# Performance work log

Measured on AMD Instinct MI355X. Metric: run time of the kernel, lower is better.

Reference implementation:

```python
import jax, jax.numpy as jnp
import numpy as np
from jax import lax

CURRICULUM_EP = 12
LI, LS, LW = 0.5, 0.8, 3.0


def _gauss_win(ws, C, dtype):
    coords = jnp.arange(ws, dtype=jnp.float32) - ws // 2
    g = jnp.exp(-coords ** 2 / (2 * 1.5 ** 2))
    win = g[None, :] * g[:, None]
    win = win / win.sum()
    # depthwise kernel, OIHW with I=1, O=C
    return jnp.broadcast_to(win[None, None], (C, 1, ws, ws)).astype(dtype)


def _dwconv(x, win, p, C):
    return lax.conv_general_dilated(
        x, win, window_strides=(1, 1), padding=[(p, p), (p, p)],
        dimension_numbers=('NCHW', 'OIHW', 'NCHW'), feature_group_count=C)


def diff_ssim(x, y, ws=11):
    C1, C2 = 0.01 ** 2, 0.03 ** 2
    C = x.shape[1]
    p = ws // 2
    win = _gauss_win(ws, C, x.dtype)
    mx = _dwconv(x, win, p, C)
    my = _dwconv(y, win, p, C)
    sxx = _dwconv(x * x, win, p, C) - mx ** 2
    syy = _dwconv(y * y, win, p, C) - my ** 2
    sxy = _dwconv(x * y, win, p, C) - mx * my
    ssim_map = (2 * mx * my + C1) * (2 * sxy + C2) / ((mx ** 2 + my ** 2 + C1) * (sxx + syy + C2))
    return ssim_map.mean()


def setup_inputs() -> dict:
    key = jax.random.key(0)
    k1, k2, k3, k4 = jax.random.split(key, 4)
    B, C, H, W = 16, 3, 512, 512
    NB = 1024  # watermark bits
    eps = 1e-4
    cover = jax.random.uniform(k1, (B, C, H, W), dtype=jnp.float32)
    wmed = jax.random.uniform(k2, (B, C, H, W), dtype=jnp.float32)
    wm_orig = jax.random.uniform(k3, (B, NB), dtype=jnp.float32)
    wm_ext = jnp.clip(jax.random.uniform(k4, (B, NB), dtype=jnp.float32), eps, 1.0 - eps)
    return {"cover": cover, "wmed": wmed, "wm_orig": wm_orig, "wm_ext": wm_ext, "epoch": 20}


def reference(cover, wmed, wm_orig, wm_ext, epoch):
    ml = jnp.mean((wmed - cover) ** 2)
    sv = diff_ssim(wmed, cover)
    sl = 1.0 - sv
    wl = jnp.mean(-(wm_orig * jnp.log(wm_ext) + (1.0 - wm_orig) * jnp.log(1.0 - wm_ext)))
    if epoch <= CURRICULUM_EP:
        w_img, w_ssim = 0.05, 0.05
    else:
        progress = min(1.0, (epoch - CURRICULUM_EP) / 10.0)
        w_img = 0.05 + (LI - 0.05) * progress
        w_ssim = 0.05 + (LS - 0.05) * progress
    total = w_img * ml + w_ssim * sl + LW * wl
    return (total, ml, sv, wl)
```

## Files before the change

### kernel.cpp

```cpp
#include <hip/hip_runtime.h>
#include <math.h>

#define H_IMG 512
#define W_IMG 512
#define TH 32
#define TW 32
#define HALO 5
#define WS11 11
#define SH (TH + 2*HALO)
#define NTHREADS 256
#define TPB 4

#define RS 36
#define RBUF_N (5*SH*RS)

typedef float f2 __attribute__((ext_vector_type(2)));

__host__ __device__ constexpr float WT(int t) {
    return (t==0||t==10) ? 0.00102838f :
           (t==1||t==9)  ? 0.00759873f :
           (t==2||t==8)  ? 0.03600075f :
           (t==3||t==7)  ? 0.10936070f :
           (t==4||t==6)  ? 0.21300556f :
           (t==5)        ? 0.26601172f : 0.0f;
}

static __device__ __forceinline__ f2 splat2(float v) { f2 r = {v, v}; return r; }

__global__ __launch_bounds__(NTHREADS, 4) void ssim_mse_tile(
        const float* __restrict__ cover, const float* __restrict__ wmed,
        float* __restrict__ part, int nParts) {
    __shared__ __align__(16) float rbuf[RBUF_N];
    __shared__ float red[8];

    const int tid = threadIdx.x;
    float ssim_acc = 0.f, mse_acc = 0.f;

    for (int it = 0; it < TPB; ++it) {
        const int tile = blockIdx.x * TPB + it;
        const int bx = tile & 15;
        const int by = (tile >> 4) & 15;
        const int pl = tile >> 8;
        const size_t pbase = (size_t)pl * (H_IMG*W_IMG);
        const float* xp = wmed + pbase;
        const float* yp = cover + pbase;
        const int ty0 = by*TH - HALO;
        const int tx0 = bx*TW - HALO;
        const bool xin = (bx != 0) && (bx != 15);

        for (int t = tid; t < SH*8; t += NTHREADS) {
            const int r = t >> 3, c0 = (t & 7) << 2;
            const int gy = ty0 + r;
            const bool rok = (unsigned)gy < (unsigned)H_IMG;
            float xv[14], yv[14];
            if (rok && xin) {
                const int ga = tx0 + c0 - 3;
                const float* rx = xp + (size_t)gy*W_IMG + ga;
                const float* ry = yp + (size_t)gy*W_IMG + ga;
                float4 XA = *(const float4*)(rx);
                float4 XB = *(const float4*)(rx + 4);
                float4 XC = *(const float4*)(rx + 8);
                float4 XD = *(const float4*)(rx + 12);
                float  XE = rx[16];
                float4 YA = *(const float4*)(ry);
                float4 YB = *(const float4*)(ry + 4);
                float4 YC = *(const float4*)(ry + 8);
                float4 YD = *(const float4*)(ry + 12);
                float  YE = ry[16];
                xv[0]=XA.w;  xv[1]=XB.x;  xv[2]=XB.y;  xv[3]=XB.z;  xv[4]=XB.w;
                xv[5]=XC.x;  xv[6]=XC.y;  xv[7]=XC.z;  xv[8]=XC.w;  xv[9]=XD.x;
                xv[10]=XD.y; xv[11]=XD.z; xv[12]=XD.w; xv[13]=XE;
                yv[0]=YA.w;  yv[1]=YB.x;  yv[2]=YB.y;  yv[3]=YB.z;  yv[4]=YB.w;
                yv[5]=YC.x;  yv[6]=YC.y;  yv[7]=YC.z;  yv[8]=YC.w;  yv[9]=YD.x;
                yv[10]=YD.y; yv[11]=YD.z; yv[12]=YD.w; yv[13]=YE;
            } else if (rok) {
                const int gc = tx0 + c0;
                const float* prx = xp + (size_t)gy*W_IMG + gc;
                const float* pry = yp + (size_t)gy*W_IMG + gc;
#pragma unroll
                for (int j = 0; j < 14; ++j) {
                    bool ok = (unsigned)(gc + j) < (unsigned)W_IMG;
                    xv[j] = ok ? prx[j] : 0.f;
                    yv[j] = ok ? pry[j] : 0.f;
                }
            } else {
#pragma unroll
                for (int j = 0; j < 14; ++j) { xv[j] = 0.f; yv[j] = 0.f; }
            }

            if (rok && r >= HALO && r < HALO+TH) {
#pragma unroll
                for (int j = 5; j < 9; ++j) {
                    float d = xv[j] - yv[j];
                    mse_acc = fmaf(d, d, mse_acc);
                }
            }

            f2 A[5][2];
#pragma unroll
            for (int f = 0; f < 5; ++f) { A[f][0] = splat2(0.f); A[f][1] = splat2(0.f); }
#pragma unroll
            for (int j = 0; j < 14; ++j) {
                float px = xv[j], py = yv[j];
                float pxx = px*px, pyy = py*py, pxy = px*py;
#pragma unroll
                for (int p = 0; p < 2; ++p) {
                    const int t0 = j - 2*p;
                    if (t0 >= 0 && t0 <= WS11) {
                        const f2 wp = {WT(t0), WT(t0-1)};
                        A[0][p] = __builtin_elementwise_fma(wp, splat2(px),  A[0][p]);
                        A[1][p] = __builtin_elementwise_fma(wp, splat2(py),  A[1][p]);
                        A[2][p] = __builtin_elementwise_fma(wp, splat2(pxx), A[2][p]);
                        A[3][p] = __builtin_elementwise_fma(wp, splat2(pyy), A[3][p]);
                        A[4][p] = __builtin_elementwise_fma(wp, splat2(pxy), A[4][p]);
                    }
                }
            }
            float* wb = &rbuf[r*RS + c0];
#pragma unroll
            for (int f = 0; f < 5; ++f) {
                *(float4*)(wb + f*SH*RS) =
                    make_float4(A[f][0].x, A[f][0].y, A[f][1].x, A[f][1].y);
            }
        }
        __syncthreads();

        if (((tid >> 7) & 1) == (it & 1)) {
            const f2 c1 = {0.01f*0.01f, 0.01f*0.01f};
            const f2 c2 = {0.03f*0.03f, 0.03f*0.03f};
            const f2 two = {2.f, 2.f};
            const int s  = tid & 127;
            const int c  = s & 31;
            const int r0 = (s >> 5) << 3;
            f2 acc2[5][4];
#pragma unroll
            for (int f = 0; f < 5; ++f)
#pragma unroll
                for (int p = 0; p < 4; ++p) acc2[f][p] = splat2(0.f);
#pragma unroll
            for (int f = 0; f < 5; ++f) {
                const float* rb = &rbuf[f*SH*RS + r0*RS + c];
#pragma unroll
                for (int i = 0; i < 18; ++i) {
                    float v = rb[i*RS];
#pragma unroll
                    for (int p = 0; p < 4; ++p) {
                        const int t0 = i - 2*p;
                        if (t0 >= 0 && t0 <= WS11) {
                            const f2 wp = {WT(t0), WT(t0-1)};
                            acc2[f][p] = __builtin_elementwise_fma(wp, splat2(v), acc2[f][p]);
                        }
                    }
                }
            }
#pragma unroll
            for (int p = 0; p < 4; ++p) {
                f2 mx = acc2[0][p], my = acc2[1][p];
                f2 sxx = acc2[2][p] - mx*mx;
                f2 syy = acc2[3][p] - my*my;
                f2 sxy = acc2[4][p] - mx*my;
                f2 num = (two*mx*my + c1) * (two*sxy + c2);
                f2 den = (mx*mx + my*my + c1) * (sxx + syy + c2);
                ssim_acc += __fdividef(num.x, den.x) + __fdividef(num.y, den.y);
            }
        }
        __syncthreads();
    }

#pragma unroll
    for (int off = 32; off > 0; off >>= 1) {
        ssim_acc += __shfl_down(ssim_acc, off);
        mse_acc  += __shfl_down(mse_acc, off);
    }
    int wid = tid >> 6, lane = tid & 63;
    if (lane == 0) { red[wid] = ssim_acc; red[4+wid] = mse_acc; }
    __syncthreads();
    if (tid == 0) {
        float s = red[0]+red[1]+red[2]+red[3];
        float m = red[4]+red[5]+red[6]+red[7];
        part[blockIdx.x] = s;
        part[nParts + blockIdx.x] = m;
    }
}

#define FT 1024
__global__ __launch_bounds__(FT) void finalize_k(
        const float* __restrict__ part, int nParts,
        const float* __restrict__ wm_orig, const float* __restrict__ wm_ext,
        int nWm, const int* __restrict__ epoch_p,
        float* __restrict__ out, double inv_npix, double inv_nwm) {
    __shared__ double red[48];
    int tid = threadIdx.x;
    double s_ssim = 0.0, s_mse = 0.0, s_wl = 0.0;
    const float4* s4 = (const float4*)part;
    const float4* m4 = (const float4*)(part + nParts);
    int n4 = nParts >> 2;
    for (int i = tid; i < n4; i += FT) {
        float4 v = s4[i];
        s_ssim += (double)((v.x + v.y) + (v.z + v.w));
        float4 u = m4[i];
        s_mse  += (double)((u.x + u.y) + (u.z + u.w));
    }
    const float4* p4 = (const float4*)wm_orig;
    const float4* q4 = (const float4*)wm_ext;
    int w4 = nWm >> 2;
    for (int i = tid; i < w4; i += FT) {
        float4 p = p4[i], q = q4[i];
        float a;
        a  = -(p.x*__logf(q.x) + (1.f-p.x)*__logf(1.f-q.x));
        a += -(p.y*__logf(q.y) + (1.f-p.y)*__logf(1.f-q.y));
        a += -(p.z*__logf(q.z) + (1.f-p.z)*__logf(1.f-q.z));
        a += -(p.w*__logf(q.w) + (1.f-p.w)*__logf(1.f-q.w));
        s_wl += (double)a;
    }
#pragma unroll
    for (int off = 32; off > 0; off >>= 1) {
        s_ssim += __shfl_down(s_ssim, off);
        s_mse  += __shfl_down(s_mse, off);
        s_wl   += __shfl_down(s_wl, off);
    }
    int wid = tid >> 6, lane = tid & 63;
    if (lane == 0) { red[wid] = s_ssim; red[16+wid] = s_mse; red[32+wid] = s_wl; }
    __syncthreads();
    if (tid == 0) {
        double ssim_sum = 0.0, mse_sum = 0.0, wl_sum = 0.0;
        for (int i = 0; i < 16; ++i) {
            ssim_sum += red[i]; mse_sum += red[16+i]; wl_sum += red[32+i];
        }
        float sv = (float)(ssim_sum * inv_npix);
        float ml = (float)(mse_sum  * inv_npix);
        float wl = (float)(wl_sum   * inv_nwm);
        int e = *epoch_p;
        float w_img, w_ssim;
        if (e <= 12) {
            w_img = 0.05f; w_ssim = 0.05f;
        } else {
            float progress = fminf(1.0f, (float)(e - 12) / 10.0f);
            w_img  = 0.05f + (0.5f - 0.05f)*progress;
            w_ssim = 0.05f + (0.8f - 0.05f)*progress;
        }
        float sl = 1.0f - sv;
        float total = w_img*ml + w_ssim*sl + 3.0f*wl;
        out[0] = total;
        out[1] = ml;
        out[2] = sv;
        out[3] = wl;
    }
}

extern "C" void kernel_launch(void* const* d_in, const int* in_sizes, int n_in,
                              void* d_out, int out_size, void* d_ws, size_t ws_size,
                              hipStream_t stream) {
    const float* cover   = (const float*)d_in[0];
    const float* wmed    = (const float*)d_in[1];
    const float* wm_orig = (const float*)d_in[2];
    const float* wm_ext  = (const float*)d_in[3];
    const int*   epoch   = (const int*)d_in[4];
    float* out = (float*)d_out;

    int npix   = in_sizes[0];
    int planes = npix / (H_IMG * W_IMG);
    int nWm    = in_sizes[2];

    int nTiles  = 16 * 16 * planes;
    int nBlocks = nTiles / TPB;
    int nParts  = nBlocks;
    float* part = (float*)d_ws;

    ssim_mse_tile<<<nBlocks, NTHREADS, 0, stream>>>(cover, wmed, part, nParts);
    finalize_k<<<1, FT, 0, stream>>>(part, nParts, wm_orig, wm_ext, nWm,
                                     epoch, out,
                                     1.0 / (double)npix, 1.0 / (double)nWm);
}
```

Before: 181.8 us.

## Stream column strips through a ring buffer to remove vertical halo recompute

Each block now walks one 32-pixel-wide column strip down an entire image plane in 32-row chunks, where before it processed four independent 32x32 tiles. Horizontal-pass results go into a 64-slot circular shared-memory buffer, so the 10 halo rows are computed and loaded once per strip instead of once per tile. This is meant to cut the redundant horizontal convolution and global loads. In exchange the grid shrinks to 16 blocks per plane with a serial 16-step chunk loop, which lowers the available parallelism and adds per-chunk barriers.

```diff
diff --git a/kernel.cpp b/kernel.cpp
--- a/kernel.cpp
+++ b/kernel.cpp
@@ -3,16 +3,15 @@
 
 #define H_IMG 512
 #define W_IMG 512
-#define TH 32
-#define TW 32
 #define HALO 5
 #define WS11 11
-#define SH (TH + 2*HALO)
 #define NTHREADS 256
-#define TPB 4
-
+#define NCHUNK 16
+
+#define SLOTS 64
 #define RS 36
-#define RBUF_N (5*SH*RS)
+#define FS (SLOTS*RS)
+#define RBUF_N (5*FS)
 
 typedef float f2 __attribute__((ext_vector_type(2)));
 
@@ -27,111 +26,127 @@
 
 static __device__ __forceinline__ f2 splat2(float v) { f2 r = {v, v}; return r; }
 
-__global__ __launch_bounds__(NTHREADS, 4) void ssim_mse_tile(
+static __device__ __forceinline__ void hconv_row(
+        const float* __restrict__ xp, const float* __restrict__ yp,
+        float* __restrict__ rbuf, int g, int c0, int bx, bool xin,
+        float& mse_acc) {
+    const bool rok = (unsigned)g < (unsigned)H_IMG;
+    const int gc = bx*32 + c0 - 5;
+    float xv[14], yv[14];
+    if (rok && xin) {
+        const int ga = gc - 3;
+        const float* rx = xp + (size_t)g*W_IMG + ga;
+        const float* ry = yp + (size_t)g*W_IMG + ga;
+        float4 XA = *(const float4*)(rx);
+        float4 XB = *(const float4*)(rx + 4);
+        float4 XC = *(const float4*)(rx + 8);
+        float4 XD = *(const float4*)(rx + 12);
+        float  XE = rx[16];
+        float4 YA = *(const float4*)(ry);
+        float4 YB = *(const float4*)(ry + 4);
+        float4 YC = *(const float4*)(ry + 8);
+        float4 YD = *(const float4*)(ry + 12);
+        float  YE = ry[16];
+        xv[0]=XA.w;  xv[1]=XB.x;  xv[2]=XB.y;  xv[3]=XB.z;  xv[4]=XB.w;
+        xv[5]=XC.x;  xv[6]=XC.y;  xv[7]=XC.z;  xv[8]=XC.w;  xv[9]=XD.x;
+        xv[10]=XD.y; xv[11]=XD.z; xv[12]=XD.w; xv[13]=XE;
+        yv[0]=YA.w;  yv[1]=YB.x;  yv[2]=YB.y;  yv[3]=YB.z;  yv[4]=YB.w;
+        yv[5]=YC.x;  yv[6]=YC.y;  yv[7]=YC.z;  yv[8]=YC.w;  yv[9]=YD.x;
+        yv[10]=YD.y; yv[11]=YD.z; yv[12]=YD.w; yv[13]=YE;
+    } else if (rok) {
+        const float* prx = xp + (size_t)g*W_IMG + gc;
+        const float* pry = yp + (size_t)g*W_IMG + gc;
+#pragma unroll
+        for (int j = 0; j < 14; ++j) {
+            bool ok = (unsigned)(gc + j) < (unsigned)W_IMG;
+            xv[j] = ok ? prx[j] : 0.f;
+            yv[j] = ok ? pry[j] : 0.f;
+        }
+    } else {
+#pragma unroll
+        for (int j = 0; j < 14; ++j) { xv[j] = 0.f; yv[j] = 0.f; }
+    }
+
+    if (rok) {
+#pragma unroll
+        for (int j = 5; j < 9; ++j) {
+            float d = xv[j] - yv[j];
+            mse_acc = fmaf(d, d, mse_acc);
+        }
+    }
+
+    f2 A[5][2];
+#pragma unroll
+    for (int f = 0; f < 5; ++f) { A[f][0] = splat2(0.f); A[f][1] = splat2(0.f); }
+#pragma unroll
+    for (int j = 0; j < 14; ++j) {
+        float px = xv[j], py = yv[j];
+        f2 vp = {px, py};
+        f2 vsq = vp * vp;
+        float pxy = px * py;
+#pragma unroll
+        for (int p = 0; p < 2; ++p) {
+            const int t0 = j - 2*p;
+            if (t0 >= 0 && t0 <= WS11) {
+                const f2 wp = {WT(t0), WT(t0-1)};
+                A[0][p] = __builtin_elementwise_fma(wp, splat2(px),    A[0][p]);
+                A[1][p] = __builtin_elementwise_fma(wp, splat2(py),    A[1][p]);
+                A[2][p] = __builtin_elementwise_fma(wp, splat2(vsq.x), A[2][p]);
+                A[3][p] = __builtin_elementwise_fma(wp, splat2(vsq.y), A[3][p]);
+                A[4][p] = __builtin_elementwise_fma(wp, splat2(pxy),   A[4][p]);
+            }
+        }
+    }
+    const int slot = (g + 5) & (SLOTS-1);
+    float* wb = &rbuf[slot*RS + c0];
+#pragma unroll
+    for (int f = 0; f < 5; ++f) {
+        *(float4*)(wb + f*FS) =
+            make_float4(A[f][0].x, A[f][0].y, A[f][1].x, A[f][1].y);
+    }
+}
+
+__global__ __launch_bounds__(NTHREADS, 3) void ssim_stream(
         const float* __restrict__ cover, const float* __restrict__ wmed,
         float* __restrict__ part, int nParts) {
     __shared__ __align__(16) float rbuf[RBUF_N];
     __shared__ float red[8];
 
     const int tid = threadIdx.x;
+    const int bx = blockIdx.x & 15;
+    const int pl = blockIdx.x >> 4;
+    const size_t pbase = (size_t)pl * (H_IMG*W_IMG);
+    const float* xp = wmed + pbase;
+    const float* yp = cover + pbase;
+    const bool xin = (bx != 0) && (bx != 15);
+
     float ssim_acc = 0.f, mse_acc = 0.f;
 
-    for (int it = 0; it < TPB; ++it) {
-        const int tile = blockIdx.x * TPB + it;
-        const int bx = tile & 15;
-        const int by = (tile >> 4) & 15;
-        const int pl = tile >> 8;
-        const size_t pbase = (size_t)pl * (H_IMG*W_IMG);
-        const float* xp = wmed + pbase;
-        const float* yp = cover + pbase;
-        const int ty0 = by*TH - HALO;
-        const int tx0 = bx*TW - HALO;
-        const bool xin = (bx != 0) && (bx != 15);
-
-        for (int t = tid; t < SH*8; t += NTHREADS) {
-            const int r = t >> 3, c0 = (t & 7) << 2;
-            const int gy = ty0 + r;
-            const bool rok = (unsigned)gy < (unsigned)H_IMG;
-            float xv[14], yv[14];
-            if (rok && xin) {
-                const int ga = tx0 + c0 - 3;
-                const float* rx = xp + (size_t)gy*W_IMG + ga;
-                const float* ry = yp + (size_t)gy*W_IMG + ga;
-                float4 XA = *(const float4*)(rx);
-                float4 XB = *(const float4*)(rx + 4);
-                float4 XC = *(const float4*)(rx + 8);
-                float4 XD = *(const float4*)(rx + 12);
-                float  XE = rx[16];
-                float4 YA = *(const float4*)(ry);
-                float4 YB = *(const float4*)(ry + 4);
-                float4 YC = *(const float4*)(ry + 8);
-                float4 YD = *(const float4*)(ry + 12);
-                float  YE = ry[16];
-                xv[0]=XA.w;  xv[1]=XB.x;  xv[2]=XB.y;  xv[3]=XB.z;  xv[4]=XB.w;
-                xv[5]=XC.x;  xv[6]=XC.y;  xv[7]=XC.z;  xv[8]=XC.w;  xv[9]=XD.x;
-                xv[10]=XD.y; xv[11]=XD.z; xv[12]=XD.w; xv[13]=XE;
-                yv[0]=YA.w;  yv[1]=YB.x;  yv[2]=YB.y;  yv[3]=YB.z;  yv[4]=YB.w;
-                yv[5]=YC.x;  yv[6]=YC.y;  yv[7]=YC.z;  yv[8]=YC.w;  yv[9]=YD.x;
-                yv[10]=YD.y; yv[11]=YD.z; yv[12]=YD.w; yv[13]=YE;
-            } else if (rok) {
-                const int gc = tx0 + c0;
-                const float* prx = xp + (size_t)gy*W_IMG + gc;
-                const float* pry = yp + (size_t)gy*W_IMG + gc;
-#pragma unroll
-                for (int j = 0; j < 14; ++j) {
-                    bool ok = (unsigned)(gc + j) < (unsigned)W_IMG;
-                    xv[j] = ok ? prx[j] : 0.f;
-                    yv[j] = ok ? pry[j] : 0.f;
-                }
-            } else {
-#pragma unroll
-                for (int j = 0; j < 14; ++j) { xv[j] = 0.f; yv[j] = 0.f; }
-            }
-
-            if (rok && r >= HALO && r < HALO+TH) {
-#pragma unroll
-                for (int j = 5; j < 9; ++j) {
-                    float d = xv[j] - yv[j];
-                    mse_acc = fmaf(d, d, mse_acc);
-                }
-            }
-
-            f2 A[5][2];
-#pragma unroll
-            for (int f = 0; f < 5; ++f) { A[f][0] = splat2(0.f); A[f][1] = splat2(0.f); }
-#pragma unroll
-            for (int j = 0; j < 14; ++j) {
-                float px = xv[j], py = yv[j];
-                float pxx = px*px, pyy = py*py, pxy = px*py;
-#pragma unroll
-                for (int p = 0; p < 2; ++p) {
-                    const int t0 = j - 2*p;
-                    if (t0 >= 0 && t0 <= WS11) {
-                        const f2 wp = {WT(t0), WT(t0-1)};
-                        A[0][p] = __builtin_elementwise_fma(wp, splat2(px),  A[0][p]);
-                        A[1][p] = __builtin_elementwise_fma(wp, splat2(py),  A[1][p]);
-                        A[2][p] = __builtin_elementwise_fma(wp, splat2(pxx), A[2][p]);
-                        A[3][p] = __builtin_elementwise_fma(wp, splat2(pyy), A[3][p]);
-                        A[4][p] = __builtin_elementwise_fma(wp, splat2(pxy), A[4][p]);
-                    }
-                }
-            }
-            float* wb = &rbuf[r*RS + c0];
-#pragma unroll
-            for (int f = 0; f < 5; ++f) {
-                *(float4*)(wb + f*SH*RS) =
-                    make_float4(A[f][0].x, A[f][0].y, A[f][1].x, A[f][1].y);
-            }
+    if (tid < 80) {
+        hconv_row(xp, yp, rbuf, (tid >> 3) - 5, (tid & 7) << 2, bx, xin, mse_acc);
+    }
+    __syncthreads();
+
+    int kbase = 0;
+#pragma clang loop unroll(disable)
+    for (int k = 0; k < NCHUNK; ++k, kbase += 32) {
+        {
+            const int r_local = tid >> 3;
+            const int c0 = (tid & 7) << 2;
+            hconv_row(xp, yp, rbuf, kbase + 5 + r_local, c0, bx, xin, mse_acc);
         }
         __syncthreads();
 
-        if (((tid >> 7) & 1) == (it & 1)) {
-            const f2 c1 = {0.01f*0.01f, 0.01f*0.01f};
-            const f2 c2 = {0.03f*0.03f, 0.03f*0.03f};
-            const f2 two = {2.f, 2.f};
+        if (((tid >> 7) & 1) == (k & 1)) {
             const int s  = tid & 127;
             const int c  = s & 31;
             const int r0 = (s >> 5) << 3;
+            int idx[18];
+#pragma unroll
+            for (int i = 0; i < 18; ++i) {
+                int sl = (kbase + r0 + i) & (SLOTS-1);
+                idx[i] = sl*RS + c;
+            }
             f2 acc2[5][4];
 #pragma unroll
             for (int f = 0; f < 5; ++f)
@@ -139,10 +154,9 @@
                 for (int p = 0; p < 4; ++p) acc2[f][p] = splat2(0.f);
 #pragma unroll
             for (int f = 0; f < 5; ++f) {
-                const float* rb = &rbuf[f*SH*RS + r0*RS + c];
 #pragma unroll
                 for (int i = 0; i < 18; ++i) {
-                    float v = rb[i*RS];
+                    float v = rbuf[f*FS + idx[i]];
 #pragma unroll
                     for (int p = 0; p < 4; ++p) {
                         const int t0 = i - 2*p;
@@ -153,6 +167,9 @@
                     }
                 }
             }
+            const f2 c1 = {0.01f*0.01f, 0.01f*0.01f};
+            const f2 c2 = {0.03f*0.03f, 0.03f*0.03f};
+            const f2 two = {2.f, 2.f};
 #pragma unroll
             for (int p = 0; p < 4; ++p) {
                 f2 mx = acc2[0][p], my = acc2[1][p];
@@ -176,9 +193,9 @@
     if (lane == 0) { red[wid] = ssim_acc; red[4+wid] = mse_acc; }
     __syncthreads();
     if (tid == 0) {
-        float s = red[0]+red[1]+red[2]+red[3];
-        float m = red[4]+red[5]+red[6]+red[7];
-        part[blockIdx.x] = s;
+        float sv = red[0]+red[1]+red[2]+red[3];
+        float m  = red[4]+red[5]+red[6]+red[7];
+        part[blockIdx.x] = sv;
         part[nParts + blockIdx.x] = m;
     }
 }
@@ -262,12 +279,11 @@
     int planes = npix / (H_IMG * W_IMG);
     int nWm    = in_sizes[2];
 
-    int nTiles  = 16 * 16 * planes;
-    int nBlocks = nTiles / TPB;
+    int nBlocks = 16 * planes;
     int nParts  = nBlocks;
     float* part = (float*)d_ws;
 
-    ssim_mse_tile<<<nBlocks, NTHREADS, 0, stream>>>(cover, wmed, part, nParts);
+    ssim_stream<<<nBlocks, NTHREADS, 0, stream>>>(cover, wmed, part, nParts);
     finalize_k<<<1, FT, 0, stream>>>(part, nParts, wm_orig, wm_ext, nWm,
                                      epoch, out,
                                      1.0 / (double)npix, 1.0 / (double)nWm);
```

Measured after the change: 193.9 us. 1.07x slower.
